# Kernel optimization log

Hardware: AMD Instinct MI355X
Metric: run time of the kernel (lower is better)

## Reference

```python
import jax, jax.numpy as jnp
import numpy as np

N_HIDDEN = 49  # number of Linear(64,64)+ReLU layers between the input and output projections
D_IN, D_HID, D_OUT = 10, 64, 10
BATCH = 1048576


def setup_inputs() -> dict:
    key = jax.random.key(0)
    ks = jax.random.split(key, 7)
    s_in = 1.0 / np.sqrt(D_IN)
    s_hid = 1.0 / np.sqrt(D_HID)
    return {
        "x": jax.random.normal(ks[0], (BATCH, D_IN), dtype=jnp.float32),
        # torch nn.Linear stores weight as [out_features, in_features]
        "w_in": jax.random.uniform(ks[1], (D_HID, D_IN), jnp.float32, -s_in, s_in),
        "b_in": jax.random.uniform(ks[2], (D_HID,), jnp.float32, -s_in, s_in),
        "w_hid": jax.random.uniform(ks[3], (N_HIDDEN, D_HID, D_HID), jnp.float32, -s_hid, s_hid),
        "b_hid": jax.random.uniform(ks[4], (N_HIDDEN, D_HID), jnp.float32, -s_hid, s_hid),
        "w_out": jax.random.uniform(ks[5], (D_OUT, D_HID), jnp.float32, -s_hid, s_hid),
        "b_out": jax.random.uniform(ks[6], (D_OUT,), jnp.float32, -s_hid, s_hid),
    }


def reference(x, w_in, b_in, w_hid, b_hid, w_out, b_out):
    # Flatten (no-op for 2D), then Linear(10,64)+ReLU
    h = jax.nn.relu(x @ w_in.T + b_in)  # [B, 64]

    def step(h, wb):
        w, b = wb
        return jax.nn.relu(h @ w.T + b), None

    h, _ = jax.lax.scan(step, h, (w_hid, b_hid))
    return h @ w_out.T + b_out  # final Linear(64,10), no activation
```

## Files before the change

kernel.cpp:

```cpp
#include <hip/hip_runtime.h>
#include <stdint.h>

typedef _Float16 half8 __attribute__((ext_vector_type(8)));
typedef __fp16 fp16x2 __attribute__((ext_vector_type(2)));
typedef float f32x16 __attribute__((ext_vector_type(16)));
typedef float f32x4  __attribute__((ext_vector_type(4)));
typedef uint32_t u32x4v __attribute__((ext_vector_type(4)));

#define NH 49

__device__ __forceinline__ uint32_t pk2(float a, float b){
  fp16x2 p = __builtin_amdgcn_cvt_pkrtz(a, b);
  return __builtin_bit_cast(uint32_t, p);
}
__device__ __forceinline__ uint32_t pk2r(float a, float b){
  fp16x2 p = __builtin_amdgcn_cvt_pkrtz(a, b);
  fp16x2 z = {(__fp16)0.f, (__fp16)0.f};
  p = __builtin_elementwise_max(p, z);
  return __builtin_bit_cast(uint32_t, p);
}

template<int RH>
__device__ __forceinline__ half8 cvt8r(const f32x16& c){
  u32x4v v;
  v.x = pk2r(c[8*RH+0], c[8*RH+1]);
  v.y = pk2r(c[8*RH+2], c[8*RH+3]);
  v.z = pk2r(c[8*RH+4], c[8*RH+5]);
  v.w = pk2r(c[8*RH+6], c[8*RH+7]);
  return __builtin_bit_cast(half8, v);
}

__device__ __forceinline__ half8 toh8(const uint32_t* d){
  union { uint32_t u[4]; half8 h; } v;
  v.u[0]=d[0]; v.u[1]=d[1]; v.u[2]=d[2]; v.u[3]=d[3];
  return v.h;
}

__device__ __forceinline__ f32x16 bias_c(const float* sbase, int mt, int hi){
  f32x16 c;
  const float* b = sbase + 32*mt + 4*hi;
  #pragma unroll
  for (int g=0; g<4; ++g){
    f32x4 v = *(const f32x4*)(b + 8*g);
    c[4*g+0]=v[0]; c[4*g+1]=v[1]; c[4*g+2]=v[2]; c[4*g+3]=v[3];
  }
  return c;
}

__device__ __forceinline__ int phi(int k){
  return (k & 51) | ((k & 4) << 1) | ((k & 8) >> 1);
}

__global__ void prep_weights(const float* __restrict__ w_in,
                             const float* __restrict__ w_hid,
                             const float* __restrict__ w_out,
                             half8* __restrict__ wf)
{
  int bid = blockIdx.x;
  int lane = threadIdx.x;
  int hi = lane >> 5, lo = lane & 31;
  half8 f;
  if (bid < 2){
    int mt = bid, row = 32*mt + lo;
    #pragma unroll
    for (int e=0; e<8; ++e){
      int k = 8*hi + e;
      f[e] = (k < 10) ? (_Float16)w_in[row*10 + k] : (_Float16)0.f;
    }
  } else if (bid < 394){
    int t = bid - 2;
    int l = t >> 3, kt = (t >> 1) & 3, mt = t & 1;
    int row = 32*mt + lo;
    #pragma unroll
    for (int e=0; e<8; ++e){
      int k = 16*kt + 8*hi + e;
      f[e] = (_Float16)w_hid[(l*64 + row)*64 + phi(k)];
    }
  } else {
    int kt = bid - 394;
    #pragma unroll
    for (int e=0; e<8; ++e){
      int k = 16*kt + 8*hi + e;
      f[e] = (lo < 10) ? (_Float16)w_out[lo*64 + phi(k)] : (_Float16)0.f;
    }
  }
  wf[bid*64 + lane] = f;
}

__device__ __forceinline__ f32x16 mfma16(half8 a, half8 b, f32x16 c){
  return __builtin_amdgcn_mfma_f32_32x32x16_f16(a, b, c, 0, 0, 0);
}

__device__ __forceinline__ void mfma_c(f32x16& d, half8 a, half8 b, const f32x16& c){
  asm("s_nop 1\n\tv_mfma_f32_32x32x16_f16 %0, %1, %2, %3"
      : "=&v"(d) : "v"(a), "v"(b), "v"(c));
}
__device__ __forceinline__ void mfma_p(f32x16& d, half8 a, half8 b){
  asm("v_mfma_f32_32x32x16_f16 %0, %1, %2, %0"
      : "+v"(d) : "v"(a), "v"(b));
}
__device__ __forceinline__ void mfma_pn(f32x16& d, half8 a, half8 b){
  asm("s_nop 1\n\tv_mfma_f32_32x32x16_f16 %0, %1, %2, %0"
      : "+v"(d) : "v"(a), "v"(b));
}

__global__ __launch_bounds__(256, 2) void mlp_fused(
    const float* __restrict__ x,
    const float* __restrict__ b_in,
    const float* __restrict__ b_hid,
    const float* __restrict__ b_out,
    const half8* __restrict__ wfrag,
    float* __restrict__ out)
{
  __shared__ __attribute__((aligned(16))) float sb[50*64 + 32];
  for (int i = threadIdx.x; i < 64; i += 256)     sb[i]      = b_in[i];
  for (int i = threadIdx.x; i < NH*64; i += 256)  sb[64 + i] = b_hid[i];
  if (threadIdx.x < 32) sb[3200 + threadIdx.x] = (threadIdx.x < 10) ? b_out[threadIdx.x] : 0.f;
  __syncthreads();

  const int lane = threadIdx.x & 63;
  const int wid  = threadIdx.x >> 6;
  const int hi   = lane >> 5;
  const int col  = lane & 31;
  const long rowbase = ((long)blockIdx.x * 4 + wid) * 128;
  const half8* whid = wfrag + 128;
  const float* sbh  = sb + 64;

  f32x16 acc[4][2];

  {
    half8 a0 = wfrag[lane];
    half8 a1 = wfrag[64 + lane];
    f32x16 cb0 = bias_c(sb, 0, hi);
    f32x16 cb1 = bias_c(sb, 1, hi);
    #pragma unroll
    for (int bt=0; bt<4; ++bt){
      const float* xr = x + (rowbase + bt*32 + col) * 10;
      float xv[8];
      if (hi == 0){
        #pragma unroll
        for (int j=0;j<8;++j) xv[j] = xr[j];
      } else {
        xv[0]=xr[8]; xv[1]=xr[9];
        #pragma unroll
        for (int j=2;j<8;++j) xv[j]=0.f;
      }
      uint32_t d[4] = { pk2(xv[0],xv[1]), pk2(xv[2],xv[3]),
                        pk2(xv[4],xv[5]), pk2(xv[6],xv[7]) };
      half8 bx = toh8(d);
      acc[bt][0] = mfma16(a0, bx, cb0);
      acc[bt][1] = mfma16(a1, bx, cb1);
    }
  }

  #pragma unroll 1
  for (int h = 0; h < NH; ++h){
    const half8* wl = whid + h*512;
    half8 w[8];
    #pragma unroll
    for (int f=0; f<8; ++f) w[f] = wl[f*64 + lane];
    const float* bl = sbh + (h << 6);
    f32x16 cb0 = bias_c(bl, 0, hi);
    f32x16 cb1 = bias_c(bl, 1, hi);

    #pragma unroll
    for (int bt=0; bt<4; ++bt){
      half8 b0 = cvt8r<0>(acc[bt][0]);
      half8 b1 = cvt8r<1>(acc[bt][0]);
      half8 b2 = cvt8r<0>(acc[bt][1]);
      half8 b3 = cvt8r<1>(acc[bt][1]);
      mfma_c (acc[bt][0], w[0], b0, cb0);
      mfma_c (acc[bt][1], w[1], b0, cb1);
      mfma_pn(acc[bt][0], w[2], b1);
      mfma_p (acc[bt][1], w[3], b1);
      mfma_pn(acc[bt][0], w[4], b2);
      mfma_p (acc[bt][1], w[5], b2);
      mfma_pn(acc[bt][0], w[6], b3);
      mfma_p (acc[bt][1], w[7], b3);
    }
  }

  const half8* wo = wfrag + 128 + 392*64;
  f32x16 cbo = bias_c(sb + 3200, 0, hi);
  f32x16 oacc[4];
  #pragma unroll
  for (int bt=0; bt<4; ++bt){
    half8 b0 = cvt8r<0>(acc[bt][0]);
    half8 b1 = cvt8r<1>(acc[bt][0]);
    half8 b2 = cvt8r<0>(acc[bt][1]);
    half8 b3 = cvt8r<1>(acc[bt][1]);
    oacc[bt] = mfma16(wo[0*64 + lane], b0, cbo);
    oacc[bt] = mfma16(wo[1*64 + lane], b1, oacc[bt]);
    oacc[bt] = mfma16(wo[2*64 + lane], b2, oacc[bt]);
    oacc[bt] = mfma16(wo[3*64 + lane], b3, oacc[bt]);
  }
  #pragma unroll
  for (int bt=0; bt<4; ++bt){
    float* orow = out + (rowbase + bt*32 + col) * 10;
    if (hi == 0){
      *(float2*)(orow + 0) = make_float2(oacc[bt][0], oacc[bt][1]);
      *(float2*)(orow + 2) = make_float2(oacc[bt][2], oacc[bt][3]);
      *(float2*)(orow + 8) = make_float2(oacc[bt][4], oacc[bt][5]);
    } else {
      *(float2*)(orow + 4) = make_float2(oacc[bt][0], oacc[bt][1]);
      *(float2*)(orow + 6) = make_float2(oacc[bt][2], oacc[bt][3]);
    }
  }
}

extern "C" void kernel_launch(void* const* d_in, const int* in_sizes, int n_in,
                              void* d_out, int out_size, void* d_ws, size_t ws_size,
                              hipStream_t stream)
{
  const float* x     = (const float*)d_in[0];
  const float* w_in  = (const float*)d_in[1];
  const float* b_in  = (const float*)d_in[2];
  const float* w_hid = (const float*)d_in[3];
  const float* b_hid = (const float*)d_in[4];
  const float* w_out = (const float*)d_in[5];
  const float* b_out = (const float*)d_in[6];
  half8* wf = (half8*)d_ws;

  prep_weights<<<398, 64, 0, stream>>>(w_in, w_hid, w_out, wf);
  mlp_fused<<<2048, 256, 0, stream>>>(x, b_in, b_hid, b_out, wf, (float*)d_out);
}
```

Measured before the change: 316.3 us.

## Halve rows per wave, raise occupancy, use builtin MFMA with setprio

Each wave now processes 64 rows instead of 128, which halves the accumulator registers. The grid doubles to 4096 blocks and launch bounds ask for 3 blocks per CU, so more waves can hide latency. The hand-written inline-asm MFMA sequence is replaced by compiler builtins wrapped in s_setprio so the compiler schedules the hazards. The trade-off is that each wave reuses its weight-fragment loads over fewer rows, so per-layer weight loads and bias reads rise relative to compute.

After: 382.3 us. 20.9% more time.

```diff
diff --git a/kernel.cpp b/kernel.cpp
--- a/kernel.cpp
+++ b/kernel.cpp
@@ -91,20 +91,7 @@
   return __builtin_amdgcn_mfma_f32_32x32x16_f16(a, b, c, 0, 0, 0);
 }
 
-__device__ __forceinline__ void mfma_c(f32x16& d, half8 a, half8 b, const f32x16& c){
-  asm("s_nop 1\n\tv_mfma_f32_32x32x16_f16 %0, %1, %2, %3"
-      : "=&v"(d) : "v"(a), "v"(b), "v"(c));
-}
-__device__ __forceinline__ void mfma_p(f32x16& d, half8 a, half8 b){
-  asm("v_mfma_f32_32x32x16_f16 %0, %1, %2, %0"
-      : "+v"(d) : "v"(a), "v"(b));
-}
-__device__ __forceinline__ void mfma_pn(f32x16& d, half8 a, half8 b){
-  asm("s_nop 1\n\tv_mfma_f32_32x32x16_f16 %0, %1, %2, %0"
-      : "+v"(d) : "v"(a), "v"(b));
-}
-
-__global__ __launch_bounds__(256, 2) void mlp_fused(
+__global__ __launch_bounds__(256, 3) void mlp_fused(
     const float* __restrict__ x,
     const float* __restrict__ b_in,
     const float* __restrict__ b_hid,
@@ -122,11 +109,11 @@
   const int wid  = threadIdx.x >> 6;
   const int hi   = lane >> 5;
   const int col  = lane & 31;
-  const long rowbase = ((long)blockIdx.x * 4 + wid) * 128;
+  const long rowbase = ((long)blockIdx.x * 4 + wid) * 64;
   const half8* whid = wfrag + 128;
   const float* sbh  = sb + 64;
 
-  f32x16 acc[4][2];
+  f32x16 acc[2][2];
 
   {
     half8 a0 = wfrag[lane];
@@ -134,7 +121,7 @@
     f32x16 cb0 = bias_c(sb, 0, hi);
     f32x16 cb1 = bias_c(sb, 1, hi);
     #pragma unroll
-    for (int bt=0; bt<4; ++bt){
+    for (int bt=0; bt<2; ++bt){
       const float* xr = x + (rowbase + bt*32 + col) * 10;
       float xv[8];
       if (hi == 0){
@@ -164,27 +151,29 @@
     f32x16 cb1 = bias_c(bl, 1, hi);
 
     #pragma unroll
-    for (int bt=0; bt<4; ++bt){
+    for (int bt=0; bt<2; ++bt){
       half8 b0 = cvt8r<0>(acc[bt][0]);
       half8 b1 = cvt8r<1>(acc[bt][0]);
       half8 b2 = cvt8r<0>(acc[bt][1]);
       half8 b3 = cvt8r<1>(acc[bt][1]);
-      mfma_c (acc[bt][0], w[0], b0, cb0);
-      mfma_c (acc[bt][1], w[1], b0, cb1);
-      mfma_pn(acc[bt][0], w[2], b1);
-      mfma_p (acc[bt][1], w[3], b1);
-      mfma_pn(acc[bt][0], w[4], b2);
-      mfma_p (acc[bt][1], w[5], b2);
-      mfma_pn(acc[bt][0], w[6], b3);
-      mfma_p (acc[bt][1], w[7], b3);
+      __builtin_amdgcn_s_setprio(1);
+      acc[bt][0] = mfma16(w[0], b0, cb0);
+      acc[bt][1] = mfma16(w[1], b0, cb1);
+      acc[bt][0] = mfma16(w[2], b1, acc[bt][0]);
+      acc[bt][1] = mfma16(w[3], b1, acc[bt][1]);
+      acc[bt][0] = mfma16(w[4], b2, acc[bt][0]);
+      acc[bt][1] = mfma16(w[5], b2, acc[bt][1]);
+      acc[bt][0] = mfma16(w[6], b3, acc[bt][0]);
+      acc[bt][1] = mfma16(w[7], b3, acc[bt][1]);
+      __builtin_amdgcn_s_setprio(0);
     }
   }
 
   const half8* wo = wfrag + 128 + 392*64;
   f32x16 cbo = bias_c(sb + 3200, 0, hi);
-  f32x16 oacc[4];
+  f32x16 oacc[2];
   #pragma unroll
-  for (int bt=0; bt<4; ++bt){
+  for (int bt=0; bt<2; ++bt){
     half8 b0 = cvt8r<0>(acc[bt][0]);
     half8 b1 = cvt8r<1>(acc[bt][0]);
     half8 b2 = cvt8r<0>(acc[bt][1]);
@@ -195,7 +184,7 @@
     oacc[bt] = mfma16(wo[3*64 + lane], b3, oacc[bt]);
   }
   #pragma unroll
-  for (int bt=0; bt<4; ++bt){
+  for (int bt=0; bt<2; ++bt){
     float* orow = out + (rowbase + bt*32 + col) * 10;
     if (hi == 0){
       *(float2*)(orow + 0) = make_float2(oacc[bt][0], oacc[bt][1]);
@@ -222,5 +211,5 @@
   half8* wf = (half8*)d_ws;
 
   prep_weights<<<398, 64, 0, stream>>>(w_in, w_hid, w_out, wf);
-  mlp_fused<<<2048, 256, 0, stream>>>(x, b_in, b_hid, b_out, wf, (float*)d_out);
-}
+  mlp_fused<<<4096, 256, 0, stream>>>(x, b_in, b_hid, b_out, wf, (float*)d_out);
+}
```
